# Kernel optimization log

Measured on AMD Instinct MI355X. Metric: run time of the kernel, lower is better.

The kernel has to match this reference:

```python
import jax, jax.numpy as jnp
import numpy as np

N_HEADS = 8
N_POINTS = 4
SPATIAL = np.array([[64, 64], [32, 32], [16, 16], [8, 8]], dtype=np.int32)


def setup_inputs() -> dict:
    key = jax.random.key(0)
    ks = jax.random.split(key, 12)
    d = 256
    H, L, P, N = N_HEADS, SPATIAL.shape[0], N_POINTS, 8
    lens = SPATIAL[:, 0] * SPATIAL[:, 1]
    Lin = int(lens.sum())
    Lq = Lin
    query = jax.random.normal(ks[0], (N, Lq, d), jnp.float32)
    reference_points = jax.random.uniform(ks[1], (N, Lq, L, 2), jnp.float32)
    input_flatten = jax.random.normal(ks[2], (N, Lin, d), jnp.float32)
    input_spatial_shapes = jnp.asarray(SPATIAL)
    starts = np.concatenate([[0], np.cumsum(lens)[:-1]]).astype(np.int32)
    input_level_start_index = jnp.asarray(starts)
    s = 1.0 / np.sqrt(d)
    W_off = jax.random.normal(ks[3], (H * L * P * 2, d), jnp.float32) * 0.01
    b_off = jax.random.normal(ks[4], (H * L * P * 2,), jnp.float32) * 0.5
    W_attn = jax.random.normal(ks[5], (H * L * P, d), jnp.float32) * 0.02
    b_attn = jnp.zeros((H * L * P,), jnp.float32)
    W_val = jax.random.normal(ks[6], (d, d), jnp.float32) * s
    b_val = jnp.zeros((d,), jnp.float32)
    W_out = jax.random.normal(ks[7], (d, d), jnp.float32) * s
    b_out = jnp.zeros((d,), jnp.float32)
    return {
        'query': query, 'reference_points': reference_points,
        'input_flatten': input_flatten,
        'input_spatial_shapes': input_spatial_shapes,
        'input_level_start_index': input_level_start_index,
        'W_off': W_off, 'b_off': b_off, 'W_attn': W_attn, 'b_attn': b_attn,
        'W_val': W_val, 'b_val': b_val, 'W_out': W_out, 'b_out': b_out,
    }


def _bilinear(img, Hl, Wl, x, y):
    # img: [B, Ch, Hl*Wl]; x, y: [B, Q, P] pixel coords (align_corners=False)
    # zero padding mode: out-of-range corners contribute 0
    x0 = jnp.floor(x)
    y0 = jnp.floor(y)
    wx = x - x0
    wy = y - y0

    def gather(xi, yi):
        valid = (xi >= 0) & (xi <= Wl - 1) & (yi >= 0) & (yi <= Hl - 1)
        ii = jnp.clip(xi, 0, Wl - 1).astype(jnp.int32)
        jj = jnp.clip(yi, 0, Hl - 1).astype(jnp.int32)
        idx = jj * Wl + ii  # [B, Q, P]
        B, Q, P = idx.shape
        v = jnp.take_along_axis(img, idx.reshape(B, 1, Q * P), axis=2)
        v = v.reshape(B, img.shape[1], Q, P)
        return v * valid[:, None].astype(img.dtype)

    return (gather(x0, y0) * ((1 - wx) * (1 - wy))[:, None]
            + gather(x0 + 1, y0) * (wx * (1 - wy))[:, None]
            + gather(x0, y0 + 1) * ((1 - wx) * wy)[:, None]
            + gather(x0 + 1, y0 + 1) * (wx * wy)[:, None])


def reference(query, reference_points, input_flatten, input_spatial_shapes,
              input_level_start_index, W_off, b_off, W_attn, b_attn,
              W_val, b_val, W_out, b_out):
    shapes = np.asarray(input_spatial_shapes)  # static structural metadata
    N, Lq, d = query.shape
    Lin = input_flatten.shape[1]
    L = shapes.shape[0]
    H, P = N_HEADS, N_POINTS
    Ch = d // H

    value = input_flatten @ W_val.T + b_val                       # [N, Lin, d]
    value = value.reshape(N, Lin, H, Ch).transpose(0, 2, 3, 1)    # [N, H, Ch, Lin]
    value = value.reshape(N * H, Ch, Lin)

    off = (query @ W_off.T + b_off).reshape(N, Lq, H, L, P, 2)
    attn = (query @ W_attn.T + b_attn).reshape(N, Lq, H, L * P)
    attn = jax.nn.softmax(attn, axis=-1).reshape(N, Lq, H, L, P)

    # normalizer is (W, H) per level
    norm = jnp.asarray(np.stack([shapes[:, 1], shapes[:, 0]], -1), query.dtype)
    loc = reference_points[:, :, None, :, None, :] + off / norm[None, None, None, :, None, :]

    attn_p = attn.transpose(0, 2, 1, 3, 4).reshape(N * H, Lq, L, P)
    starts = np.concatenate([[0], np.cumsum(shapes[:, 0] * shapes[:, 1])])

    out = jnp.zeros((N * H, Ch, Lq), query.dtype)
    for l in range(L):
        Hl, Wl = int(shapes[l, 0]), int(shapes[l, 1])
        v_l = value[:, :, starts[l]:starts[l + 1]]                # [B, Ch, Hl*Wl]
        g = loc[:, :, :, l].transpose(0, 2, 1, 3, 4).reshape(N * H, Lq, P, 2)
        # grid_sample align_corners=False with grid=2*loc-1 -> pixel = loc*W - 0.5
        x = g[..., 0] * Wl - 0.5
        y = g[..., 1] * Hl - 0.5
        samp = _bilinear(v_l, Hl, Wl, x, y)                       # [B, Ch, Lq, P]
        out = out + jnp.einsum('bcqp,bqp->bcq', samp, attn_p[:, :, l])

    out = out.reshape(N, H, Ch, Lq).transpose(0, 3, 1, 2).reshape(N, Lq, d)
    return out @ W_out.T + b_out
```

## Files before the change

### kernel.cpp

```cpp
#include <hip/hip_runtime.h>
#include <hip/hip_bf16.h>

#define NQ   5440
#define NB   8
#define DIM  256
#define NH   8
#define CHN  32
#define NLV  4
#define NPT  4
#define MTOT (NB * NQ)

typedef __attribute__((ext_vector_type(8))) short s16x8;
typedef __attribute__((ext_vector_type(4))) short s16x4;
typedef __attribute__((ext_vector_type(4))) float f32x4;
typedef unsigned short ushort_t;

#define WVAL 0
#define WOFF 65536
#define WATT 131072
#define WOUT 163840
#define WTOT 229376

__device__ __forceinline__ short f2bf(float x) {
    union { __hip_bfloat16 b; short s; } u;
    u.b = __float2bfloat16(x);
    return u.s;
}

__global__ __launch_bounds__(256) void cvt_weights(const float* __restrict__ wv,
                                                   const float* __restrict__ wo,
                                                   const float* __restrict__ wa,
                                                   const float* __restrict__ wu,
                                                   ushort_t* __restrict__ wb) {
    int i = (blockIdx.x * 256 + threadIdx.x) * 4;
    if (i >= WTOT) return;
    const float* src;
    int off;
    if (i < WOFF)       { src = wv; off = WVAL; }
    else if (i < WATT)  { src = wo; off = WOFF; }
    else if (i < WOUT)  { src = wa; off = WATT; }
    else                { src = wu; off = WOUT; }
    f32x4 v = *(const f32x4*)(src + (i - off));
    s16x4 b;
#pragma unroll
    for (int e = 0; e < 4; ++e) b[e] = f2bf(v[e]);
    *(s16x4*)(wb + i) = b;
}

#define LDSK 72

__device__ __forceinline__ void stC(float* p, float v) { *p = v; }
__device__ __forceinline__ void stC(ushort_t* p, float v) { *(short*)p = f2bf(v); }

template <typename AT, typename CT>
__device__ __forceinline__ void gemm_core(const AT* __restrict__ A,
                                          const ushort_t* __restrict__ Wt,
                                          const float* __restrict__ biasT,
                                          CT* __restrict__ Ct, int ldC, int rowBase) {
    __shared__ short As[128 * LDSK];
    __shared__ short Ws[128 * LDSK];

    const int t = threadIdx.x;
    const int lane = t & 63, wave = t >> 6;
    const int wm = wave >> 1, wn = wave & 1;
    const int lr = lane & 15, quad = lane >> 4;

    f32x4 acc[4][4];
#pragma unroll
    for (int i = 0; i < 4; ++i)
#pragma unroll
        for (int j = 0; j < 4; ++j)
#pragma unroll
            for (int r = 0; r < 4; ++r) acc[i][j][r] = 0.f;

    f32x4 pf0[4], pf1[4];
    s16x8 pb[4];
    s16x8 pw[4];

#pragma unroll
    for (int i = 0; i < 4; ++i) {
        int c = t + i * 256, r = c >> 3, kc = (c & 7) * 8;
        const AT* pa = A + (size_t)(rowBase + r) * DIM + kc;
        if constexpr (sizeof(AT) == 4) {
            pf0[i] = *(const f32x4*)pa;
            pf1[i] = *(const f32x4*)(pa + 4);
        } else {
            pb[i] = *(const s16x8*)pa;
        }
        pw[i] = *(const s16x8*)(Wt + (size_t)r * DIM + kc);
    }

    for (int ks = 0; ks < 4; ++ks) {
        if (ks) __syncthreads();
#pragma unroll
        for (int i = 0; i < 4; ++i) {
            int c = t + i * 256, r = c >> 3, kc = (c & 7) * 8;
            s16x8 av;
            if constexpr (sizeof(AT) == 4) {
#pragma unroll
                for (int e = 0; e < 4; ++e) {
                    av[e] = f2bf(pf0[i][e]);
                    av[e + 4] = f2bf(pf1[i][e]);
                }
            } else {
                av = pb[i];
            }
            *(s16x8*)&As[r * LDSK + kc] = av;
            *(s16x8*)&Ws[r * LDSK + kc] = pw[i];
        }
        if (ks < 3) {
            const int k0 = (ks + 1) * 64;
#pragma unroll
            for (int i = 0; i < 4; ++i) {
                int c = t + i * 256, r = c >> 3, kc = (c & 7) * 8;
                const AT* pa = A + (size_t)(rowBase + r) * DIM + k0 + kc;
                if constexpr (sizeof(AT) == 4) {
                    pf0[i] = *(const f32x4*)pa;
                    pf1[i] = *(const f32x4*)(pa + 4);
                } else {
                    pb[i] = *(const s16x8*)pa;
                }
                pw[i] = *(const s16x8*)(Wt + (size_t)r * DIM + k0 + kc);
            }
        }
        __syncthreads();
#pragma unroll
        for (int kk = 0; kk < 64; kk += 32) {
            s16x8 afr[4], wfr[4];
#pragma unroll
            for (int i = 0; i < 4; ++i)
                afr[i] = *(const s16x8*)&As[(wm * 64 + i * 16 + lr) * LDSK + kk + quad * 8];
#pragma unroll
            for (int j = 0; j < 4; ++j)
                wfr[j] = *(const s16x8*)&Ws[(wn * 64 + j * 16 + lr) * LDSK + kk + quad * 8];
#pragma unroll
            for (int i = 0; i < 4; ++i)
#pragma unroll
                for (int j = 0; j < 4; ++j)
                    acc[i][j] = __builtin_amdgcn_mfma_f32_16x16x32_bf16(
                        afr[i], wfr[j], acc[i][j], 0, 0, 0);
        }
    }

    float bj[4];
#pragma unroll
    for (int j = 0; j < 4; ++j) bj[j] = biasT[wn * 64 + j * 16 + lr];
#pragma unroll
    for (int i = 0; i < 4; ++i)
#pragma unroll
        for (int r = 0; r < 4; ++r) {
            int row = rowBase + wm * 64 + i * 16 + quad * 4 + r;
#pragma unroll
            for (int j = 0; j < 4; ++j) {
                int col = wn * 64 + j * 16 + lr;
                stC(&Ct[(size_t)row * ldC + col], acc[i][j][r] + bj[j]);
            }
        }
}

__global__ __launch_bounds__(256) void gemm_fused(const float* __restrict__ inputf,
                                                  const float* __restrict__ query,
                                                  const ushort_t* __restrict__ wb,
                                                  const float* __restrict__ b_val,
                                                  const float* __restrict__ b_off,
                                                  const float* __restrict__ b_attn,
                                                  ushort_t* __restrict__ v_val,
                                                  float* __restrict__ v_off,
                                                  float* __restrict__ v_attn) {
    const int gy = blockIdx.y;
    const int rowBase = blockIdx.x * 128;
    if (gy < 2)
        gemm_core<float, ushort_t>(inputf, wb + WVAL + (size_t)gy * 128 * DIM,
                                   b_val + gy * 128, v_val + gy * 128, DIM, rowBase);
    else if (gy < 4)
        gemm_core<float, float>(query, wb + WOFF + (size_t)(gy - 2) * 128 * DIM,
                                b_off + (gy - 2) * 128, v_off + (gy - 2) * 128, DIM,
                                rowBase);
    else
        gemm_core<float, float>(query, wb + WATT, b_attn, v_attn, 128, rowBase);
}

__global__ __launch_bounds__(256) void gemm_out(const ushort_t* __restrict__ A,
                                                const ushort_t* __restrict__ wb,
                                                const float* __restrict__ bias,
                                                float* __restrict__ C) {
    gemm_core<ushort_t, float>(A, wb + WOUT + (size_t)blockIdx.y * 128 * DIM,
                               bias + blockIdx.y * 128, C + blockIdx.y * 128, DIM,
                               blockIdx.x * 128);
}

__global__ __launch_bounds__(256) void sample_kernel(
    const float* __restrict__ refp,
    const float* __restrict__ off,
    const float* __restrict__ attn,
    const ushort_t* __restrict__ valb,
    const int* __restrict__ shapes,
    const int* __restrict__ starts,
    ushort_t* __restrict__ sampb)
{
    const int qBase = blockIdx.x * 8;
    const int t = threadIdx.x;

    __shared__ __align__(16) int   sidx[1024][4];
    __shared__ __align__(16) float sww[1024][4];

#pragma unroll
    for (int it = 0; it < 4; ++it) {
        const int i = t + it * 256;
        const int q8 = i >> 7, hlp = i & 127;
        const int h = hlp >> 4, lp = hlp & 15, l = lp >> 2;
        const int q = qBase + q8;
        const int n = q / NQ;
        const int Wl = shapes[2 * l + 1], Hl = shapes[2 * l];
        const float Wf = (float)Wl, Hf = (float)Hl;
        const float2 rp = *(const float2*)(refp + ((size_t)q * NLV + l) * 2);
        const float2 oo = *(const float2*)(off + (size_t)q * DIM + h * 32 + lp * 2);
        const float x = (rp.x + oo.x / Wf) * Wf - 0.5f;
        const float y = (rp.y + oo.y / Hf) * Hf - 0.5f;

        float logit = attn[(size_t)q * 128 + h * 16 + lp];
        float m = logit;
#pragma unroll
        for (int s = 8; s >= 1; s >>= 1) m = fmaxf(m, __shfl_xor(m, s, 16));
        float e = __expf(logit - m);
        float ss = e;
#pragma unroll
        for (int s = 8; s >= 1; s >>= 1) ss += __shfl_xor(ss, s, 16);
        const float aw = e / ss;

        const float xf = floorf(x), yf = floorf(y);
        const int ix = (int)xf, iy = (int)yf;
        const float wx = x - xf, wy = y - yf;
        const int ix1 = ix + 1, iy1 = iy + 1;
        const bool bx0 = (ix >= 0) & (ix < Wl);
        const bool bx1 = (ix1 >= 0) & (ix1 < Wl);
        const bool by0 = (iy >= 0) & (iy < Hl);
        const bool by1 = (iy1 >= 0) & (iy1 < Hl);
        const int cx0 = min(max(ix, 0), Wl - 1), cx1 = min(max(ix1, 0), Wl - 1);
        const int cy0 = min(max(iy, 0), Hl - 1), cy1 = min(max(iy1, 0), Hl - 1);
        const int base = n * NQ + starts[l];
        int4 id;
        id.x = (base + cy0 * Wl + cx0) << 9;
        id.y = (base + cy0 * Wl + cx1) << 9;
        id.z = (base + cy1 * Wl + cx0) << 9;
        id.w = (base + cy1 * Wl + cx1) << 9;
        f32x4 w;
        w[0] = (bx0 && by0) ? aw * (1.f - wx) * (1.f - wy) : 0.f;
        w[1] = (bx1 && by0) ? aw * wx * (1.f - wy) : 0.f;
        w[2] = (bx0 && by1) ? aw * (1.f - wx) * wy : 0.f;
        w[3] = (bx1 && by1) ? aw * wx * wy : 0.f;
        *(int4*)sidx[i] = id;
        *(f32x4*)sww[i] = w;
    }
    __syncthreads();

    const int q8 = t >> 5, r = t & 31;
    const int h = r >> 2, cg = r & 3;
    const int q = qBase + q8;
    const char* vb = (const char*)valb + h * 64 + cg * 16;

    f32x4 acc0, acc1;
    acc0[0] = acc0[1] = acc0[2] = acc0[3] = 0.f;
    acc1[0] = acc1[1] = acc1[2] = acc1[3] = 0.f;
#pragma unroll
    for (int j = 0; j < 16; ++j) {
        const int lp = (j + h) & 15;
        const int slot = (q8 << 7) + (h << 4) + lp;
        const int4 id = *(const int4*)sidx[slot];
        const f32x4 w = *(const f32x4*)sww[slot];
        const uint4 u0 = *(const uint4*)(vb + (size_t)(unsigned)id.x);
        const uint4 u1 = *(const uint4*)(vb + (size_t)(unsigned)id.y);
        const uint4 u2 = *(const uint4*)(vb + (size_t)(unsigned)id.z);
        const uint4 u3 = *(const uint4*)(vb + (size_t)(unsigned)id.w);
#define ACC8(u, wgt)                                                          \
        {                                                                     \
            f32x4 lo, hi;                                                     \
            lo[0] = __uint_as_float(u.x << 16);                               \
            lo[1] = __uint_as_float(u.x & 0xffff0000u);                       \
            lo[2] = __uint_as_float(u.y << 16);                               \
            lo[3] = __uint_as_float(u.y & 0xffff0000u);                       \
            hi[0] = __uint_as_float(u.z << 16);                               \
            hi[1] = __uint_as_float(u.z & 0xffff0000u);                       \
            hi[2] = __uint_as_float(u.w << 16);                               \
            hi[3] = __uint_as_float(u.w & 0xffff0000u);                       \
            acc0 += lo * (wgt);                                               \
            acc1 += hi * (wgt);                                               \
        }
        ACC8(u0, w[0]);
        ACC8(u1, w[1]);
        ACC8(u2, w[2]);
        ACC8(u3, w[3]);
#undef ACC8
    }
    s16x8 o;
#pragma unroll
    for (int e = 0; e < 4; ++e) {
        o[e] = f2bf(acc0[e]);
        o[e + 4] = f2bf(acc1[e]);
    }
    *(s16x8*)(sampb + (size_t)q * DIM + h * CHN + cg * 8) = o;
}

extern "C" void kernel_launch(void* const* d_in, const int* in_sizes, int n_in,
                              void* d_out, int out_size, void* d_ws, size_t ws_size,
                              hipStream_t stream) {
    const float* query  = (const float*)d_in[0];
    const float* refp   = (const float*)d_in[1];
    const float* inputf = (const float*)d_in[2];
    const int* shapes   = (const int*)d_in[3];
    const int* starts   = (const int*)d_in[4];
    const float* W_off  = (const float*)d_in[5];
    const float* b_off  = (const float*)d_in[6];
    const float* W_attn = (const float*)d_in[7];
    const float* b_attn = (const float*)d_in[8];
    const float* W_val  = (const float*)d_in[9];
    const float* b_val  = (const float*)d_in[10];
    const float* W_out  = (const float*)d_in[11];
    const float* b_out  = (const float*)d_in[12];
    float* out = (float*)d_out;

    char* ws = (char*)d_ws;
    ushort_t* wb     = (ushort_t*)ws;
    ushort_t* v_val  = (ushort_t*)(ws + 512 * 1024);
    float*    v_off  = (float*)(ws + 512 * 1024 + (size_t)MTOT * DIM * 2);
    float*    v_attn = (float*)((char*)v_off + (size_t)MTOT * DIM * 4);
    ushort_t* sampb  = (ushort_t*)((char*)v_attn + (size_t)MTOT * 128 * 4);

    dim3 blk(256);
    cvt_weights<<<dim3(WTOT / 1024), blk, 0, stream>>>(W_val, W_off, W_attn, W_out, wb);
    gemm_fused<<<dim3(MTOT / 128, 5), blk, 0, stream>>>(inputf, query, wb, b_val,
                                                        b_off, b_attn, v_val, v_off,
                                                        v_attn);
    sample_kernel<<<dim3(MTOT / 8), blk, 0, stream>>>(refp, v_off, v_attn, v_val,
                                                      shapes, starts, sampb);
    gemm_out<<<dim3(MTOT / 128, 2), blk, 0, stream>>>(sampb, wb, b_out, out);
}
```

Baseline: 279.5 us.

## Pre-convert activations to bf16, use direct global-to-LDS loads, fp16 packed sampling

Adds a pre-pass that converts the input and query activations to bf16 alongside the weights. The GEMM core then loads tiles straight into LDS with global_load_lds, using an XOR-style swizzled layout in place of register staging and a padded layout. The value projection is now stored as fp16, and the sampling kernel accumulates with packed half2 FMAs, flushing to fp32 every four points. The sampling block size is halved to 128 threads. These changes trade an extra conversion pass and its memory traffic, plus lower fp16 accumulation precision, for less conversion work inside the GEMMs and cheaper sampling arithmetic.

```diff
diff --git a/kernel.cpp b/kernel.cpp
--- a/kernel.cpp
+++ b/kernel.cpp
@@ -1,5 +1,6 @@
 #include <hip/hip_runtime.h>
 #include <hip/hip_bf16.h>
+#include <hip/hip_fp16.h>
 
 #define NQ   5440
 #define NB   8
@@ -27,42 +28,60 @@
     return u.s;
 }
 
-__global__ __launch_bounds__(256) void cvt_weights(const float* __restrict__ wv,
-                                                   const float* __restrict__ wo,
-                                                   const float* __restrict__ wa,
-                                                   const float* __restrict__ wu,
-                                                   ushort_t* __restrict__ wb) {
-    int i = (blockIdx.x * 256 + threadIdx.x) * 4;
-    if (i >= WTOT) return;
-    const float* src;
-    int off;
-    if (i < WOFF)       { src = wv; off = WVAL; }
-    else if (i < WATT)  { src = wo; off = WOFF; }
-    else if (i < WOUT)  { src = wa; off = WATT; }
-    else                { src = wu; off = WOUT; }
-    f32x4 v = *(const f32x4*)(src + (i - off));
-    s16x4 b;
-#pragma unroll
-    for (int e = 0; e < 4; ++e) b[e] = f2bf(v[e]);
-    *(s16x4*)(wb + i) = b;
-}
-
-#define LDSK 72
+__device__ __forceinline__ void gload_lds16(const void* g, void* l) {
+    __builtin_amdgcn_global_load_lds(
+        (const __attribute__((address_space(1))) unsigned int*)g,
+        (__attribute__((address_space(3))) unsigned int*)l, 16, 0, 0);
+}
+
+__device__ __forceinline__ void cvt8b(const float* s, ushort_t* d) {
+    f32x4 a = *(const f32x4*)s, b = *(const f32x4*)(s + 4);
+    s16x8 v;
+#pragma unroll
+    for (int e = 0; e < 4; ++e) { v[e] = f2bf(a[e]); v[e + 4] = f2bf(b[e]); }
+    *(s16x8*)d = v;
+}
+
+__global__ __launch_bounds__(256) void cvt_all(const float* __restrict__ inputf,
+                                               const float* __restrict__ query,
+                                               const float* __restrict__ wv,
+                                               const float* __restrict__ wo,
+                                               const float* __restrict__ wa,
+                                               const float* __restrict__ wu,
+                                               ushort_t* __restrict__ binf,
+                                               ushort_t* __restrict__ bq,
+                                               ushort_t* __restrict__ wb) {
+    const int i = (blockIdx.x * 256 + threadIdx.x) * 8;
+    if (blockIdx.y == 0) {
+        cvt8b(inputf + i, binf + i);
+    } else if (blockIdx.y == 1) {
+        cvt8b(query + i, bq + i);
+    } else {
+        if (i >= WTOT) return;
+        const float* src;
+        int off;
+        if (i < WOFF)      { src = wv; off = WVAL; }
+        else if (i < WATT) { src = wo; off = WOFF; }
+        else if (i < WOUT) { src = wa; off = WATT; }
+        else               { src = wu; off = WOUT; }
+        cvt8b(src + (i - off), wb + i);
+    }
+}
 
 __device__ __forceinline__ void stC(float* p, float v) { *p = v; }
-__device__ __forceinline__ void stC(ushort_t* p, float v) { *(short*)p = f2bf(v); }
-
-template <typename AT, typename CT>
-__device__ __forceinline__ void gemm_core(const AT* __restrict__ A,
+__device__ __forceinline__ void stC(__half* p, float v) { *p = __float2half(v); }
+
+template <typename CT>
+__device__ __forceinline__ void gemm_core(const ushort_t* __restrict__ A,
                                           const ushort_t* __restrict__ Wt,
                                           const float* __restrict__ biasT,
                                           CT* __restrict__ Ct, int ldC, int rowBase) {
-    __shared__ short As[128 * LDSK];
-    __shared__ short Ws[128 * LDSK];
+    __shared__ ushort_t As[128 * 64];
+    __shared__ ushort_t Ws[128 * 64];
 
     const int t = threadIdx.x;
-    const int lane = t & 63, wave = t >> 6;
-    const int wm = wave >> 1, wn = wave & 1;
+    const int lane = t & 63, w = t >> 6;
+    const int wm = w >> 1, wn = w & 1;
     const int lr = lane & 15, quad = lane >> 4;
 
     f32x4 acc[4][4];
@@ -72,67 +91,35 @@
         for (int j = 0; j < 4; ++j)
 #pragma unroll
             for (int r = 0; r < 4; ++r) acc[i][j][r] = 0.f;
-
-    f32x4 pf0[4], pf1[4];
-    s16x8 pb[4];
-    s16x8 pw[4];
-
-#pragma unroll
-    for (int i = 0; i < 4; ++i) {
-        int c = t + i * 256, r = c >> 3, kc = (c & 7) * 8;
-        const AT* pa = A + (size_t)(rowBase + r) * DIM + kc;
-        if constexpr (sizeof(AT) == 4) {
-            pf0[i] = *(const f32x4*)pa;
-            pf1[i] = *(const f32x4*)(pa + 4);
-        } else {
-            pb[i] = *(const s16x8*)pa;
-        }
-        pw[i] = *(const s16x8*)(Wt + (size_t)r * DIM + kc);
-    }
 
     for (int ks = 0; ks < 4; ++ks) {
         if (ks) __syncthreads();
 #pragma unroll
         for (int i = 0; i < 4; ++i) {
-            int c = t + i * 256, r = c >> 3, kc = (c & 7) * 8;
-            s16x8 av;
-            if constexpr (sizeof(AT) == 4) {
-#pragma unroll
-                for (int e = 0; e < 4; ++e) {
-                    av[e] = f2bf(pf0[i][e]);
-                    av[e + 4] = f2bf(pf1[i][e]);
-                }
-            } else {
-                av = pb[i];
-            }
-            *(s16x8*)&As[r * LDSK + kc] = av;
-            *(s16x8*)&Ws[r * LDSK + kc] = pw[i];
-        }
-        if (ks < 3) {
-            const int k0 = (ks + 1) * 64;
-#pragma unroll
-            for (int i = 0; i < 4; ++i) {
-                int c = t + i * 256, r = c >> 3, kc = (c & 7) * 8;
-                const AT* pa = A + (size_t)(rowBase + r) * DIM + k0 + kc;
-                if constexpr (sizeof(AT) == 4) {
-                    pf0[i] = *(const f32x4*)pa;
-                    pf1[i] = *(const f32x4*)(pa + 4);
-                } else {
-                    pb[i] = *(const s16x8*)pa;
-                }
-                pw[i] = *(const s16x8*)(Wt + (size_t)r * DIM + k0 + kc);
-            }
+            const int c = t + i * 256;
+            const int r = c >> 3, s = c & 7;
+            const int g = (s - r) & 7;
+            const int ke = ks * 64 + g * 8;
+            gload_lds16(A + (size_t)(rowBase + r) * DIM + ke,
+                        &As[(size_t)(i * 256 + w * 64) * 8]);
+            gload_lds16(Wt + (size_t)r * DIM + ke,
+                        &Ws[(size_t)(i * 256 + w * 64) * 8]);
         }
         __syncthreads();
 #pragma unroll
         for (int kk = 0; kk < 64; kk += 32) {
             s16x8 afr[4], wfr[4];
-#pragma unroll
-            for (int i = 0; i < 4; ++i)
-                afr[i] = *(const s16x8*)&As[(wm * 64 + i * 16 + lr) * LDSK + kk + quad * 8];
-#pragma unroll
-            for (int j = 0; j < 4; ++j)
-                wfr[j] = *(const s16x8*)&Ws[(wn * 64 + j * 16 + lr) * LDSK + kk + quad * 8];
+            const int G = (kk >> 3) + quad;
+#pragma unroll
+            for (int i = 0; i < 4; ++i) {
+                const int R = wm * 64 + i * 16 + lr;
+                afr[i] = *(const s16x8*)&As[(R * 8 + ((G + R) & 7)) * 8];
+            }
+#pragma unroll
+            for (int j = 0; j < 4; ++j) {
+                const int R = wn * 64 + j * 16 + lr;
+                wfr[j] = *(const s16x8*)&Ws[(R * 8 + ((G + R) & 7)) * 8];
+            }
 #pragma unroll
             for (int i = 0; i < 4; ++i)
 #pragma unroll
@@ -158,58 +145,57 @@
         }
 }
 
-__global__ __launch_bounds__(256) void gemm_fused(const float* __restrict__ inputf,
-                                                  const float* __restrict__ query,
+__global__ __launch_bounds__(256) void gemm_fused(const ushort_t* __restrict__ binf,
+                                                  const ushort_t* __restrict__ bq,
                                                   const ushort_t* __restrict__ wb,
                                                   const float* __restrict__ b_val,
                                                   const float* __restrict__ b_off,
                                                   const float* __restrict__ b_attn,
-                                                  ushort_t* __restrict__ v_val,
+                                                  __half* __restrict__ bval,
                                                   float* __restrict__ v_off,
                                                   float* __restrict__ v_attn) {
     const int gy = blockIdx.y;
     const int rowBase = blockIdx.x * 128;
     if (gy < 2)
-        gemm_core<float, ushort_t>(inputf, wb + WVAL + (size_t)gy * 128 * DIM,
-                                   b_val + gy * 128, v_val + gy * 128, DIM, rowBase);
+        gemm_core<__half>(binf, wb + WVAL + (size_t)gy * 128 * DIM,
+                          b_val + gy * 128, bval + gy * 128, DIM, rowBase);
     else if (gy < 4)
-        gemm_core<float, float>(query, wb + WOFF + (size_t)(gy - 2) * 128 * DIM,
-                                b_off + (gy - 2) * 128, v_off + (gy - 2) * 128, DIM,
-                                rowBase);
+        gemm_core<float>(bq, wb + WOFF + (size_t)(gy - 2) * 128 * DIM,
+                         b_off + (gy - 2) * 128, v_off + (gy - 2) * 128, DIM, rowBase);
     else
-        gemm_core<float, float>(query, wb + WATT, b_attn, v_attn, 128, rowBase);
+        gemm_core<float>(bq, wb + WATT, b_attn, v_attn, 128, rowBase);
 }
 
 __global__ __launch_bounds__(256) void gemm_out(const ushort_t* __restrict__ A,
                                                 const ushort_t* __restrict__ wb,
                                                 const float* __restrict__ bias,
                                                 float* __restrict__ C) {
-    gemm_core<ushort_t, float>(A, wb + WOUT + (size_t)blockIdx.y * 128 * DIM,
-                               bias + blockIdx.y * 128, C + blockIdx.y * 128, DIM,
-                               blockIdx.x * 128);
-}
-
-__global__ __launch_bounds__(256) void sample_kernel(
+    gemm_core<float>(A, wb + WOUT + (size_t)blockIdx.y * 128 * DIM,
+                     bias + blockIdx.y * 128, C + blockIdx.y * 128, DIM,
+                     blockIdx.x * 128);
+}
+
+__global__ __launch_bounds__(128) void sample_kernel(
     const float* __restrict__ refp,
     const float* __restrict__ off,
     const float* __restrict__ attn,
-    const ushort_t* __restrict__ valb,
+    const __half* __restrict__ bval,
     const int* __restrict__ shapes,
     const int* __restrict__ starts,
     ushort_t* __restrict__ sampb)
 {
-    const int qBase = blockIdx.x * 8;
+    const int qBase = blockIdx.x * 4;
     const int t = threadIdx.x;
 
-    __shared__ __align__(16) int   sidx[1024][4];
-    __shared__ __align__(16) float sww[1024][4];
+    __shared__ __align__(16) int     sidx[512][4];
+    __shared__ __align__(16) __half2 sww[512][4];
 
 #pragma unroll
     for (int it = 0; it < 4; ++it) {
-        const int i = t + it * 256;
-        const int q8 = i >> 7, hlp = i & 127;
+        const int i = t + it * 128;
+        const int q4 = i >> 7, hlp = i & 127;
         const int h = hlp >> 4, lp = hlp & 15, l = lp >> 2;
-        const int q = qBase + q8;
+        const int q = qBase + q4;
         const int n = q / NQ;
         const int Wl = shapes[2 * l + 1], Hl = shapes[2 * l];
         const float Wf = (float)Wl, Hf = (float)Hl;
@@ -244,60 +230,57 @@
         id.y = (base + cy0 * Wl + cx1) << 9;
         id.z = (base + cy1 * Wl + cx0) << 9;
         id.w = (base + cy1 * Wl + cx1) << 9;
-        f32x4 w;
-        w[0] = (bx0 && by0) ? aw * (1.f - wx) * (1.f - wy) : 0.f;
-        w[1] = (bx1 && by0) ? aw * wx * (1.f - wy) : 0.f;
-        w[2] = (bx0 && by1) ? aw * (1.f - wx) * wy : 0.f;
-        w[3] = (bx1 && by1) ? aw * wx * wy : 0.f;
+        __half2 wp[4];
+        wp[0] = __float2half2_rn((bx0 && by0) ? aw * (1.f - wx) * (1.f - wy) : 0.f);
+        wp[1] = __float2half2_rn((bx1 && by0) ? aw * wx * (1.f - wy) : 0.f);
+        wp[2] = __float2half2_rn((bx0 && by1) ? aw * (1.f - wx) * wy : 0.f);
+        wp[3] = __float2half2_rn((bx1 && by1) ? aw * wx * wy : 0.f);
         *(int4*)sidx[i] = id;
-        *(f32x4*)sww[i] = w;
+        *(uint4*)&sww[i][0] = *(uint4*)wp;
     }
     __syncthreads();
 
-    const int q8 = t >> 5, r = t & 31;
+    const int q4 = t >> 5, r = t & 31;
     const int h = r >> 2, cg = r & 3;
-    const int q = qBase + q8;
-    const char* vb = (const char*)valb + h * 64 + cg * 16;
-
-    f32x4 acc0, acc1;
-    acc0[0] = acc0[1] = acc0[2] = acc0[3] = 0.f;
-    acc1[0] = acc1[1] = acc1[2] = acc1[3] = 0.f;
+    const int q = qBase + q4;
+    const char* vb = (const char*)bval + h * 64 + cg * 16;
+
+    __half2 acch[4];
+    float accf[8];
+#pragma unroll
+    for (int e = 0; e < 4; ++e) acch[e] = __float2half2_rn(0.f);
+#pragma unroll
+    for (int e = 0; e < 8; ++e) accf[e] = 0.f;
+
 #pragma unroll
     for (int j = 0; j < 16; ++j) {
         const int lp = (j + h) & 15;
-        const int slot = (q8 << 7) + (h << 4) + lp;
+        const int slot = (q4 << 7) + (h << 4) + lp;
         const int4 id = *(const int4*)sidx[slot];
-        const f32x4 w = *(const f32x4*)sww[slot];
-        const uint4 u0 = *(const uint4*)(vb + (size_t)(unsigned)id.x);
-        const uint4 u1 = *(const uint4*)(vb + (size_t)(unsigned)id.y);
-        const uint4 u2 = *(const uint4*)(vb + (size_t)(unsigned)id.z);
-        const uint4 u3 = *(const uint4*)(vb + (size_t)(unsigned)id.w);
-#define ACC8(u, wgt)                                                          \
-        {                                                                     \
-            f32x4 lo, hi;                                                     \
-            lo[0] = __uint_as_float(u.x << 16);                               \
-            lo[1] = __uint_as_float(u.x & 0xffff0000u);                       \
-            lo[2] = __uint_as_float(u.y << 16);                               \
-            lo[3] = __uint_as_float(u.y & 0xffff0000u);                       \
-            hi[0] = __uint_as_float(u.z << 16);                               \
-            hi[1] = __uint_as_float(u.z & 0xffff0000u);                       \
-            hi[2] = __uint_as_float(u.w << 16);                               \
-            hi[3] = __uint_as_float(u.w & 0xffff0000u);                       \
-            acc0 += lo * (wgt);                                               \
-            acc1 += hi * (wgt);                                               \
-        }
-        ACC8(u0, w[0]);
-        ACC8(u1, w[1]);
-        ACC8(u2, w[2]);
-        ACC8(u3, w[3]);
-#undef ACC8
+        uint4 wu = *(const uint4*)&sww[slot][0];
+        const __half2* wp = (const __half2*)&wu;
+        int idc[4] = {id.x, id.y, id.z, id.w};
+#pragma unroll
+        for (int c = 0; c < 4; ++c) {
+            const uint4 u = *(const uint4*)(vb + (size_t)(unsigned)idc[c]);
+            const __half2* hv = (const __half2*)&u;
+#pragma unroll
+            for (int e = 0; e < 4; ++e) acch[e] = __hfma2(hv[e], wp[c], acch[e]);
+        }
+        if ((j & 3) == 3) {
+#pragma unroll
+            for (int e = 0; e < 4; ++e) {
+                float2 f = __half22float2(acch[e]);
+                accf[2 * e] += f.x;
+                accf[2 * e + 1] += f.y;
+                acch[e] = __float2half2_rn(0.f);
+            }
+        }
     }
+
     s16x8 o;
 #pragma unroll
-    for (int e = 0; e < 4; ++e) {
-        o[e] = f2bf(acc0[e]);
-        o[e + 4] = f2bf(acc1[e]);
-    }
+    for (int e = 0; e < 8; ++e) o[e] = f2bf(accf[e]);
     *(s16x8*)(sampb + (size_t)q * DIM + h * CHN + cg * 8) = o;
 }
 
@@ -319,19 +302,21 @@
     const float* b_out  = (const float*)d_in[12];
     float* out = (float*)d_out;
 
+    const size_t AB = (size_t)MTOT * DIM * 2;
     char* ws = (char*)d_ws;
-    ushort_t* wb     = (ushort_t*)ws;
-    ushort_t* v_val  = (ushort_t*)(ws + 512 * 1024);
-    float*    v_off  = (float*)(ws + 512 * 1024 + (size_t)MTOT * DIM * 2);
-    float*    v_attn = (float*)((char*)v_off + (size_t)MTOT * DIM * 4);
-    ushort_t* sampb  = (ushort_t*)((char*)v_attn + (size_t)MTOT * 128 * 4);
-
-    dim3 blk(256);
-    cvt_weights<<<dim3(WTOT / 1024), blk, 0, stream>>>(W_val, W_off, W_attn, W_out, wb);
-    gemm_fused<<<dim3(MTOT / 128, 5), blk, 0, stream>>>(inputf, query, wb, b_val,
-                                                        b_off, b_attn, v_val, v_off,
-                                                        v_attn);
-    sample_kernel<<<dim3(MTOT / 8), blk, 0, stream>>>(refp, v_off, v_attn, v_val,
-                                                      shapes, starts, sampb);
-    gemm_out<<<dim3(MTOT / 128, 2), blk, 0, stream>>>(sampb, wb, b_out, out);
-}
+    ushort_t* wb    = (ushort_t*)ws;
+    ushort_t* binf  = (ushort_t*)(ws + 512 * 1024);
+    ushort_t* bq    = (ushort_t*)(ws + 512 * 1024 + AB);
+    __half*   bval  = (__half*)(ws + 512 * 1024 + 2 * AB);
+    float*    v_off = (float*)(ws + 512 * 1024 + 3 * AB);
+    float*    v_attn= (float*)(ws + 512 * 1024 + 3 * AB + (size_t)MTOT * DIM * 4);
+    ushort_t* sampb = binf;
+
+    cvt_all<<<dim3(MTOT * DIM / 2048, 3), dim3(256), 0, stream>>>(
+        inputf, query, W_val, W_off, W_attn, W_out, binf, bq, wb);
+    gemm_fused<<<dim3(MTOT / 128, 5), dim3(256), 0, stream>>>(
+        binf, bq, wb, b_val, b_off, b_attn, bval, v_off, v_attn);
+    sample_kernel<<<dim3(MTOT / 4), dim3(128), 0, stream>>>(
+        refp, v_off, v_attn, bval, shapes, starts, sampb);
+    gemm_out<<<dim3(MTOT / 128, 2), dim3(256), 0, stream>>>(sampb, wb, b_out, out);
+}
```

After: 278.0 us. No clear change (-0.6%).
